# Optimization experiments

Measured on AMD Instinct MI355X. Metric: run time of the kernel, lower is better.

The kernel has to match this reference:

```python
import jax, jax.numpy as jnp
import numpy as np

D_FEAT = 6
T = 64
HID = 128
N = 8192
EPS = 1e-5


def setup_inputs() -> dict:
    key = jax.random.key(0)
    ks = jax.random.split(key, 16)
    s = 0.08
    rn = lambda k, shape: jax.random.normal(k, shape, dtype=jnp.float32) * s
    return {
        "x": jax.random.normal(ks[0], (N, D_FEAT * T), dtype=jnp.float32),
        "w_ih0": rn(ks[1], (3 * HID, D_FEAT)),
        "w_hh0": rn(ks[2], (3 * HID, HID)),
        "b_ih0": rn(ks[3], (3 * HID,)),
        "b_hh0": rn(ks[4], (3 * HID,)),
        "w_ih1": rn(ks[5], (3 * HID, HID)),
        "w_hh1": rn(ks[6], (3 * HID, HID)),
        "b_ih1": rn(ks[7], (3 * HID,)),
        "b_hh1": rn(ks[8], (3 * HID,)),
        "bn1_g": jnp.ones((HID,), jnp.float32),
        "bn1_b": jnp.zeros((HID,), jnp.float32),
        "fc_w": rn(ks[9], (HID, HID)),
        "fc_b": rn(ks[10], (HID,)),
        "bn2_g": jnp.ones((HID,), jnp.float32),
        "bn2_b": jnp.zeros((HID,), jnp.float32),
        "fco_w": rn(ks[11], (1, HID)),
        "fco_b": rn(ks[12], (1,)),
    }


def _gru_layer(xs, w_ih, w_hh, b_ih, b_hh):
    # xs: [T, N, in] -> per-step hidden states [T, N, H] (torch nn.GRU math)
    H = w_hh.shape[1]
    gi_all = jnp.einsum('tni,gi->tng', xs, w_ih) + b_ih  # precompute input gates [T,N,3H]

    def step(h, gi):
        gh = h @ w_hh.T + b_hh
        i_r, i_z, i_n = jnp.split(gi, 3, axis=1)
        h_r, h_z, h_n = jnp.split(gh, 3, axis=1)
        r = jax.nn.sigmoid(i_r + h_r)
        z = jax.nn.sigmoid(i_z + h_z)
        n = jnp.tanh(i_n + r * h_n)
        h_new = (1.0 - z) * n + z * h
        return h_new, h_new

    h0 = jnp.zeros((xs.shape[1], H), dtype=xs.dtype)
    _, hs = jax.lax.scan(step, h0, gi_all)
    return hs


def _bn(x, g, b):
    # BatchNorm1d with track_running_stats=False: always uses batch stats
    mu = jnp.mean(x, axis=0)
    var = jnp.mean((x - mu) ** 2, axis=0)
    return (x - mu) * jax.lax.rsqrt(var + EPS) * g + b


def reference(x, w_ih0, w_hh0, b_ih0, b_hh0, w_ih1, w_hh1, b_ih1, b_hh1,
              bn1_g, bn1_b, fc_w, fc_b, bn2_g, bn2_b, fco_w, fco_b):
    n = x.shape[0]
    # reshape(N, d_feat, T).permute(0,2,1) -> time-major [T, N, d_feat] for scan
    xs = x.reshape(n, D_FEAT, T).transpose(2, 0, 1)
    h1 = _gru_layer(xs, w_ih0, w_hh0, b_ih0, b_hh0)
    h2 = _gru_layer(h1, w_ih1, w_hh1, b_ih1, b_hh1)
    hidden = _bn(h2[-1], bn1_g, bn1_b)  # [N, H]
    # cal_attention: mean_d(h_i * h_j) - mean(h_i)*mean(h_j)
    #   == (hidden @ hidden.T)/H - outer(row_means, row_means)  (exact identity)
    m = jnp.mean(hidden, axis=1)
    att = hidden @ hidden.T / jnp.float32(hidden.shape[1]) - jnp.outer(m, m)  # [N, N]
    out = att @ hidden              # [N, H]
    out = out @ fc_w.T + fc_b
    out = _bn(out, bn2_g, bn2_b)
    out = jax.nn.leaky_relu(out, 0.01)
    return (out @ fco_w.T + fco_b).squeeze(-1)  # [N]
```

## Files before the change

kernel.cpp:

```cpp
#include <hip/hip_runtime.h>

typedef unsigned short u16;
typedef short bf16x8 __attribute__((ext_vector_type(8)));
typedef float f32x4 __attribute__((ext_vector_type(4)));

#define NBATCH 8192

__device__ __forceinline__ f32x4 mfma16(bf16x8 a, bf16x8 b, f32x4 c) {
  return __builtin_amdgcn_mfma_f32_16x16x32_bf16(a, b, c, 0, 0, 0);
}
__device__ __forceinline__ u16 f2bf(float f) {
  unsigned int u = __float_as_uint(f);
  return (u16)((u + 0x7FFFu + ((u >> 16) & 1u)) >> 16);
}
__device__ __forceinline__ float bf2f(u16 h) {
  return __uint_as_float(((unsigned int)h) << 16);
}
__device__ __forceinline__ float sigm(float x) {
  return __builtin_amdgcn_rcpf(1.f + __builtin_amdgcn_exp2f(-1.44269504f * x));
}
__device__ __forceinline__ float tanh_(float x) {
  float t = __builtin_amdgcn_exp2f(2.88539008f * x);
  return 1.f - 2.f * __builtin_amdgcn_rcpf(t + 1.f);
}
__device__ __forceinline__ bf16x8 pack8(const float* p) {
  float4 a = *(const float4*)p, b = *(const float4*)(p + 4);
  bf16x8 r;
  r[0] = (short)f2bf(a.x); r[1] = (short)f2bf(a.y);
  r[2] = (short)f2bf(a.z); r[3] = (short)f2bf(a.w);
  r[4] = (short)f2bf(b.x); r[5] = (short)f2bf(b.y);
  r[6] = (short)f2bf(b.z); r[7] = (short)f2bf(b.w);
  return r;
}

__device__ __forceinline__ void step_barrier() {
  __builtin_amdgcn_sched_barrier(0);
  asm volatile("s_waitcnt lgkmcnt(0)" ::: "memory");
  __builtin_amdgcn_s_barrier();
  __builtin_amdgcn_sched_barrier(0);
}

#define A_H0B  0
#define A_XB   8192
#define A_LDS  10240

#define GRU0_STEP(RD, WR, T)                                                    \
  {                                                                             \
    if (xact && (T) < 63) {                                                     \
      u16 xh = f2bf(xv);                                                        \
      u16 xl = f2bf(xv - bf2f(xh));                                             \
      char* xw = sm + A_XB + (WR)*1024 + xm*64 + xd*2;                          \
      *(u16*)xw = xh; *(u16*)(xw + 16) = xl; *(u16*)(xw + 32) = xh;             \
      if ((T) < 62) xv = gx[(T) + 2];                                           \
    }                                                                           \
    f32x4 accr = {brzr, brzr, brzr, brzr};                                      \
    f32x4 accz = {brzz, brzz, brzz, brzz};                                      \
    f32x4 acch = {bhn0, bhn0, bhn0, bhn0};                                      \
    f32x4 acci = {bin0, bin0, bin0, bin0};                                      \
    _Pragma("unroll") for (int ki = 0; ki < 4; ++ki) {                          \
      bf16x8 a0 = *(bf16x8*)(sm + A_H0B + (RD)*4096 + arow0 + ad[ki]);          \
      accr = mfma16(a0, wr0[ki], accr);                                         \
      accz = mfma16(a0, wz0[ki], accz);                                         \
      acch = mfma16(a0, wn0[ki], acch);                                         \
    }                                                                           \
    {                                                                           \
      bf16x8 ax0 = *(bf16x8*)(sm + A_XB + (RD)*1024 + xr0);                     \
      accr = mfma16(ax0, wf0a, accr);                                           \
      accz = mfma16(ax0, wf0b, accz);                                           \
      acci = mfma16(ax0, wf0c, acci);                                           \
    }                                                                           \
    if ((T) >= 1) {       \
      uint2 gv = *(const uint2*)(sm + A_H0B + (RD)*4096 + tid*8);               \
      *(uint2*)(h0seq + (size_t)((T)-1)*2097152 + gofs) = gv;                   \
    }                                                                           \
    _Pragma("unroll") for (int r = 0; r < 4; ++r) {                             \
      float rr = sigm(accr[r]);                                                 \
      float zz = sigm(accz[r]);                                                 \
      float nn = tanh_(__builtin_fmaf(rr, acch[r], acci[r]));                   \
      float h = h0s[r]; h = __builtin_fmaf(zz, h - nn, nn); h0s[r] = h;         \
      *(u16*)(sm + A_H0B + (WR)*4096 + st[r]) = f2bf(h);                        \
    }                                                                           \
    step_barrier();                                                             \
  }

__global__ __attribute__((amdgpu_flat_work_group_size(512, 512)))
void k_gru0(const float* __restrict__ x,
            const float* __restrict__ wih0, const float* __restrict__ whh0,
            const float* __restrict__ bih0, const float* __restrict__ bhh0,
            char* __restrict__ h0seq) {
  extern __shared__ char sm[];
  const int tid = threadIdx.x;
  const int wid = tid >> 6;
  const int lane = tid & 63;
  const int lq = lane >> 4;
  const int ul = lane & 15;
  const int u  = wid * 16 + ul;
  const int n0 = blockIdx.x * 16;
  const int sx = (ul & 7) << 4;
  const int gofs = blockIdx.x * 4096 + tid * 8;

  for (int idx = tid; idx < 2560; idx += 512)
    *(float*)(sm + A_H0B + idx * 4) = 0.f;

  bf16x8 wr0[4], wz0[4], wn0[4];
#pragma unroll
  for (int ki = 0; ki < 4; ++ki) {
    wr0[ki] = pack8(whh0 + u * 128 + ki * 32 + lq * 8);
    wz0[ki] = pack8(whh0 + (128 + u) * 128 + ki * 32 + lq * 8);
    wn0[ki] = pack8(whh0 + (256 + u) * 128 + ki * 32 + lq * 8);
  }

  bf16x8 wf0a, wf0b, wf0c;
  {
    u16 t0[8] = {0,0,0,0,0,0,0,0}, t1[8] = {0,0,0,0,0,0,0,0}, t2[8] = {0,0,0,0,0,0,0,0};
    u16* ts[3] = {t0, t1, t2};
#pragma unroll
    for (int i = 0; i < 3; ++i) {
      int g = u + 128 * i;
      if (lq < 2) {
        for (int d = 0; d < 6; ++d) ts[i][d] = f2bf(wih0[g * 6 + d]);
      } else if (lq == 2) {
        for (int d = 0; d < 6; ++d) {
          float w = wih0[g * 6 + d];
          u16 h = f2bf(w);
          ts[i][d] = f2bf(w - bf2f(h));
        }
      }
    }
    wf0a = *(bf16x8*)t0; wf0b = *(bf16x8*)t1; wf0c = *(bf16x8*)t2;
  }
  const float brzr = bih0[u] + bhh0[u];
  const float brzz = bih0[u + 128] + bhh0[u + 128];
  const float bin0 = bih0[u + 256], bhn0 = bhh0[u + 256];

  int ad[4];
#pragma unroll
  for (int ki = 0; ki < 4; ++ki) ad[ki] = (ki * 64 + lq * 16) ^ sx;
  const int arow0 = ul * 256;
  const int xr0 = ul * 64 + lq * 16;
  int st[4];
#pragma unroll
  for (int r = 0; r < 4; ++r) {
    int m = lq * 4 + r;
    st[r] = m * 256 + ((u * 2) ^ ((m & 7) << 4));
  }

  float h0s[4];
#pragma unroll
  for (int r = 0; r < 4; ++r) h0s[r] = 0.f;

  const int xm = tid / 6, xd = tid - 6 * xm;
  const bool xact = tid < 96;
  const float* gx = x + (size_t)(n0 + xm) * 384 + xd * 64;

  __syncthreads();

  float xv = 0.f;
  if (xact) {
    float x0 = gx[0];
    u16 h = f2bf(x0);
    u16 l = f2bf(x0 - bf2f(h));
    char* p = sm + A_XB + xm * 64 + xd * 2;
    *(u16*)p = h; *(u16*)(p + 16) = l; *(u16*)(p + 32) = h;
    xv = gx[1];
  }
  __syncthreads();

  for (int t = 0; t < 64; t += 2) {
    GRU0_STEP(0, 1, t)
    GRU0_STEP(1, 0, t + 1)
  }
  {
    uint2 gv = *(const uint2*)(sm + A_H0B + tid * 8);
    *(uint2*)(h0seq + (size_t)63 * 2097152 + gofs) = gv;
  }
}

#define B_H0IN 0
#define B_H1B  8192
#define B_LDS  16384

#define GRU1_STEP(RD, WR, T)                                                    \
  {                                                                             \
    uint2 hvnew = {0u, 0u};                                                     \
    if ((T) < 62) hvnew = *(const uint2*)(gsrc + (size_t)((T)+2)*2097152);      \
    f32x4 accr = {brzr, brzr, brzr, brzr};                                      \
    f32x4 accz = {brzz, brzz, brzz, brzz};                                      \
    f32x4 acci = {bin1, bin1, bin1, bin1};                                      \
    f32x4 acch = {bhn1, bhn1, bhn1, bhn1};                                      \
    _Pragma("unroll") for (int ki = 0; ki < 4; ++ki) {                          \
      bf16x8 p0 = *(bf16x8*)(sm + B_H0IN + (RD)*4096 + arow0 + ad[ki]);         \
      bf16x8 q0 = *(bf16x8*)(sm + B_H1B + (RD)*4096 + arow0 + ad[ki]);          \
      accr = mfma16(p0, wih1f[0][ki], accr);                                    \
      accr = mfma16(q0, wr1[ki], accr);                                         \
      accz = mfma16(p0, wih1f[1][ki], accz);                                    \
      accz = mfma16(q0, wz1[ki], accz);                                         \
      acci = mfma16(p0, wih1f[2][ki], acci);                                    \
      acch = mfma16(q0, wn1[ki], acch);                                         \
    }                                                                           \
    if ((T) < 63) *(uint2*)(sm + B_H0IN + (WR)*4096 + tid*8) = pend;            \
    _Pragma("unroll") for (int r = 0; r < 4; ++r) {                             \
      float rr = sigm(accr[r]);                                                 \
      float zz = sigm(accz[r]);                                                 \
      float nn = tanh_(__builtin_fmaf(rr, acch[r], acci[r]));                   \
      float h = h1s[r]; h = __builtin_fmaf(zz, h - nn, nn); h1s[r] = h;         \
      *(u16*)(sm + B_H1B + (WR)*4096 + st[r]) = f2bf(h);                        \
    }                                                                           \
    step_barrier();                                                             \
    pend = hvnew;                                                               \
  }

__global__ __attribute__((amdgpu_flat_work_group_size(512, 512)))
void k_gru1(const float* __restrict__ wih1, const float* __restrict__ whh1,
            const float* __restrict__ bih1, const float* __restrict__ bhh1,
            const char* __restrict__ h0seq, float* __restrict__ hraw) {
  extern __shared__ char sm[];
  const int tid = threadIdx.x;
  const int wid = tid >> 6;
  const int lane = tid & 63;
  const int lq = lane >> 4;
  const int ul = lane & 15;
  const int u  = wid * 16 + ul;
  const int n0 = blockIdx.x * 16;
  const int sx = (ul & 7) << 4;
  const char* gsrc = h0seq + blockIdx.x * 4096 + tid * 8;

  for (int idx = tid; idx < 1024; idx += 512)
    *(float*)(sm + B_H1B + idx * 4) = 0.f;
  {
    uint2 h0v = *(const uint2*)(gsrc);
    *(uint2*)(sm + B_H0IN + tid * 8) = h0v;
  }
  uint2 pend = *(const uint2*)(gsrc + 2097152);

  bf16x8 wih1f[3][4], wr1[4], wz1[4], wn1[4];
#pragma unroll
  for (int i = 0; i < 3; ++i) {
    int g = u + 128 * i;
#pragma unroll
    for (int ki = 0; ki < 4; ++ki)
      wih1f[i][ki] = pack8(wih1 + g * 128 + ki * 32 + lq * 8);
  }
#pragma unroll
  for (int ki = 0; ki < 4; ++ki) {
    wr1[ki] = pack8(whh1 + u * 128 + ki * 32 + lq * 8);
    wz1[ki] = pack8(whh1 + (128 + u) * 128 + ki * 32 + lq * 8);
    wn1[ki] = pack8(whh1 + (256 + u) * 128 + ki * 32 + lq * 8);
  }

  const float brzr = bih1[u] + bhh1[u];
  const float brzz = bih1[u + 128] + bhh1[u + 128];
  const float bin1 = bih1[u + 256], bhn1 = bhh1[u + 256];

  int ad[4];
#pragma unroll
  for (int ki = 0; ki < 4; ++ki) ad[ki] = (ki * 64 + lq * 16) ^ sx;
  const int arow0 = ul * 256;
  int st[4];
#pragma unroll
  for (int r = 0; r < 4; ++r) {
    int m = lq * 4 + r;
    st[r] = m * 256 + ((u * 2) ^ ((m & 7) << 4));
  }

  float h1s[4];
#pragma unroll
  for (int r = 0; r < 4; ++r) h1s[r] = 0.f;

  __syncthreads();

  for (int t = 0; t < 64; t += 2) {
    GRU1_STEP(0, 1, t)
    GRU1_STEP(1, 0, t + 1)
  }

#pragma unroll
  for (int r = 0; r < 4; ++r) {
    int m = lq * 4 + r;
    hraw[(size_t)(n0 + m) * 128 + u] = h1s[r];
  }
}

__global__ void k_bn1p(const float* __restrict__ hraw, float* __restrict__ p) {
  __shared__ float s0[256], s1[256];
  int tid = threadIdx.x, b = blockIdx.x;
  int f = tid & 127, r = tid >> 7;
  float s = 0.f, q = 0.f;
  for (int n = b * 64 + r; n < b * 64 + 64; n += 2) {
    float v = hraw[(size_t)n * 128 + f];
    s += v; q += v * v;
  }
  s0[tid] = s; s1[tid] = q;
  __syncthreads();
  if (tid < 128) {
    p[b * 256 + tid] = s0[tid] + s0[tid + 128];
    p[b * 256 + 128 + tid] = s1[tid] + s1[tid + 128];
  }
}

__global__ void k_bn1r(const float* __restrict__ p, float* __restrict__ mu1,
                       float* __restrict__ rs1) {
  int f = threadIdx.x;
  float s = 0.f, q = 0.f;
  for (int b = 0; b < 128; ++b) { s += p[b * 256 + f]; q += p[b * 256 + 128 + f]; }
  float mu = s / 8192.f, var = q / 8192.f - mu * mu;
  mu1[f] = mu; rs1[f] = rsqrtf(var + 1e-5f);
}

__global__ void k_attp(const float* __restrict__ hraw, const float* __restrict__ mu1,
                       const float* __restrict__ rs1, const float* __restrict__ g1,
                       const float* __restrict__ b1, float* __restrict__ hidden,
                       float* __restrict__ mvec, float* __restrict__ gpart,
                       float* __restrict__ mhpart) {
  __shared__ float hid[64][128];
  __shared__ float mld[64];
  int tid = threadIdx.x, blk = blockIdx.x, n0 = blk * 64;
  for (int idx = tid; idx < 64 * 128; idx += 256) {
    int n = idx >> 7, f = idx & 127;
    float v = (hraw[(size_t)(n0 + n) * 128 + f] - mu1[f]) * rs1[f] * g1[f] + b1[f];
    hid[n][f] = v;
    hidden[(size_t)(n0 + n) * 128 + f] = v;
  }
  __syncthreads();
  if (tid < 64) {
    float s = 0.f;
    for (int f = 0; f < 128; ++f) s += hid[tid][f];
    s *= (1.f / 128.f);
    mld[tid] = s; mvec[n0 + tid] = s;
  }
  __syncthreads();
  int i = tid >> 1, j0 = (tid & 1) * 64;
  float acc[64];
#pragma unroll
  for (int j = 0; j < 64; ++j) acc[j] = 0.f;
  for (int n = 0; n < 64; ++n) {
    float a = hid[n][i];
#pragma unroll
    for (int j = 0; j < 64; ++j) acc[j] += a * hid[n][j0 + j];
  }
#pragma unroll
  for (int j = 0; j < 64; ++j) gpart[(size_t)blk * 16384 + i * 128 + j0 + j] = acc[j];
  if (tid < 128) {
    float s = 0.f;
    for (int n = 0; n < 64; ++n) s += mld[n] * hid[n][tid];
    mhpart[blk * 128 + tid] = s;
  }
}

__global__ void k_attfa(const float* __restrict__ gpart, const float* __restrict__ mhpart,
                        float* __restrict__ gfull, float* __restrict__ mhfull) {
  int idx = blockIdx.x * 256 + threadIdx.x;
  float s = 0.f;
  for (int b = 0; b < 128; ++b) s += gpart[(size_t)b * 16384 + idx];
  gfull[idx] = s;
  if (blockIdx.x == 0 && threadIdx.x < 128) {
    float t = 0.f;
    for (int b = 0; b < 128; ++b) t += mhpart[b * 128 + threadIdx.x];
    mhfull[threadIdx.x] = t;
  }
}

__global__ void k_attfb(const float* __restrict__ gfull, const float* __restrict__ mhfull,
                        const float* __restrict__ fcw, float* __restrict__ m2,
                        float* __restrict__ uvec) {
  int idx = blockIdx.x * 128 + threadIdx.x;
  int k = idx >> 7, j = idx & 127;
  const float4* ga = (const float4*)(gfull + k * 128);
  const float4* fb = (const float4*)(fcw + j * 128);
  float a0 = 0.f, a1 = 0.f, a2 = 0.f, a3 = 0.f;
#pragma unroll 8
  for (int f = 0; f < 32; ++f) {
    float4 a = ga[f], b = fb[f];
    a0 += a.x * b.x; a1 += a.y * b.y; a2 += a.z * b.z; a3 += a.w * b.w;
  }
  m2[idx] = (a0 + a1 + a2 + a3) * (1.f / 128.f);
  if (idx < 128) {
    float s = 0.f;
    const float* fr = fcw + idx * 128;
#pragma unroll 8
    for (int f = 0; f < 128; ++f) s += mhfull[f] * fr[f];
    uvec[idx] = s;
  }
}

__global__ void k_out2(const float* __restrict__ hidden, const float* __restrict__ mvec,
                       const float* __restrict__ m2g, const float* __restrict__ uvec,
                       const float* __restrict__ fcb, float* __restrict__ out2,
                       float* __restrict__ bn2p) {
  extern __shared__ char smo[];
  float* m2l = (float*)smo;
  float* hl = m2l + 16384;
  float* ml = hl + 4096;
  float* red = ml + 32;
  int tid = threadIdx.x, blk = blockIdx.x, n0 = blk * 32;
  for (int idx = tid; idx < 16384; idx += 256) m2l[idx] = m2g[idx];
  for (int idx = tid; idx < 4096; idx += 256) hl[idx] = hidden[(size_t)n0 * 128 + idx];
  if (tid < 32) ml[tid] = mvec[n0 + tid];
  __syncthreads();
  int j = tid & 127, rg = tid >> 7;
  float uj = uvec[j], bj = fcb[j];
  float s1 = 0.f, s2 = 0.f;
  for (int q = 0; q < 16; ++q) {
    int nl = rg * 16 + q;
    float s = bj - ml[nl] * uj;
    const float* hr = hl + nl * 128;
#pragma unroll 8
    for (int k = 0; k < 128; ++k) s += hr[k] * m2l[k * 128 + j];
    out2[(size_t)(n0 + nl) * 128 + j] = s;
    s1 += s; s2 += s * s;
  }
  red[tid] = s1; red[256 + tid] = s2;
  __syncthreads();
  if (tid < 128) {
    bn2p[blk * 256 + tid] = red[tid] + red[128 + tid];
    bn2p[blk * 256 + 128 + tid] = red[256 + tid] + red[384 + tid];
  }
}

__global__ void k_bn2(const float* __restrict__ bn2p, float* __restrict__ mu2,
                      float* __restrict__ rs2) {
  int j = threadIdx.x;
  float s = 0.f, q = 0.f;
  for (int b = 0; b < 256; ++b) {
    s += bn2p[b * 256 + j];
    q += bn2p[b * 256 + 128 + j];
  }
  float mu = s / 8192.f, var = q / 8192.f - mu * mu;
  mu2[j] = mu; rs2[j] = rsqrtf(var + 1e-5f);
}

__global__ void k_fin(const float* __restrict__ out2, const float* __restrict__ mu2,
                      const float* __restrict__ rs2, const float* __restrict__ g2,
                      const float* __restrict__ b2, const float* __restrict__ fcow,
                      const float* __restrict__ fcob, float* __restrict__ y) {
  int tid = threadIdx.x, lane = tid & 63, w = tid >> 6;
  int n = blockIdx.x * 4 + w;
  float s = 0.f;
#pragma unroll
  for (int h = 0; h < 2; ++h) {
    int j = lane + h * 64;
    float v = (out2[(size_t)n * 128 + j] - mu2[j]) * rs2[j] * g2[j] + b2[j];
    v = fmaxf(v, 0.01f * v);
    s += v * fcow[j];
  }
  for (int off = 32; off; off >>= 1) s += __shfl_down(s, off);
  if (!lane) y[n] = s + fcob[0];
}

extern "C" void kernel_launch(void* const* d_in, const int* in_sizes, int n_in,
                              void* d_out, int out_size, void* d_ws, size_t ws_size,
                              hipStream_t stream) {
  const float* x    = (const float*)d_in[0];
  const float* wih0 = (const float*)d_in[1];
  const float* whh0 = (const float*)d_in[2];
  const float* bih0 = (const float*)d_in[3];
  const float* bhh0 = (const float*)d_in[4];
  const float* wih1 = (const float*)d_in[5];
  const float* whh1 = (const float*)d_in[6];
  const float* bih1 = (const float*)d_in[7];
  const float* bhh1 = (const float*)d_in[8];
  const float* g1   = (const float*)d_in[9];
  const float* b1   = (const float*)d_in[10];
  const float* fcw  = (const float*)d_in[11];
  const float* fcb  = (const float*)d_in[12];
  const float* g2   = (const float*)d_in[13];
  const float* b2   = (const float*)d_in[14];
  const float* fcow = (const float*)d_in[15];
  const float* fcob = (const float*)d_in[16];

  char* ws = (char*)d_ws;
  float* hraw   = (float*)(ws + 0);
  float* hidden = (float*)(ws + 4194304);
  float* mvec   = (float*)(ws + 8388608);
  float* mu1    = (float*)(ws + 8421376);
  float* rs1    = (float*)(ws + 8421888);
  float* gpart  = (float*)(ws + 8422400);
  float* mhpart = (float*)(ws + 16811008);
  float* m2     = (float*)(ws + 16876544);
  float* uvec   = (float*)(ws + 16942080);
  float* out2   = (float*)(ws + 16942592);
  float* bn2p   = (float*)(ws + 21136896);
  float* mu2    = (float*)(ws + 21399040);
  float* rs2    = (float*)(ws + 21399552);
  float* gfull  = (float*)(ws + 21400064);
  float* mhfull = (float*)(ws + 21465600);
  char*  h0seq  = (char*)(ws + 21495808);

  (void)hipFuncSetAttribute((const void*)k_out2,
                            hipFuncAttributeMaxDynamicSharedMemorySize, 84096);

  k_gru0<<<512, 512, A_LDS, stream>>>(x, wih0, whh0, bih0, bhh0, h0seq);
  k_gru1<<<512, 512, B_LDS, stream>>>(wih1, whh1, bih1, bhh1, h0seq, hraw);
  k_bn1p<<<128, 256, 0, stream>>>(hraw, bn2p);
  k_bn1r<<<1, 128, 0, stream>>>(bn2p, mu1, rs1);
  k_attp<<<128, 256, 0, stream>>>(hraw, mu1, rs1, g1, b1, hidden, mvec, gpart, mhpart);
  k_attfa<<<64, 256, 0, stream>>>(gpart, mhpart, gfull, mhfull);
  k_attfb<<<128, 128, 0, stream>>>(gfull, mhfull, fcw, m2, uvec);
  k_out2<<<256, 256, 84096, stream>>>(hidden, mvec, m2, uvec, fcb, out2, bn2p);
  k_bn2<<<1, 128, 0, stream>>>(bn2p, mu2, rs2);
  k_fin<<<2048, 256, 0, stream>>>(out2, mu2, rs2, g2, b2, fcow, fcob, (float*)d_out);
}
```

Measured before the change: 332.7 us.

## Load GRU1 layer-0 inputs directly from global in MFMA layout and fuse BN1 partials

GRU0 now writes each step's hidden state to global in a row-major, de-swizzled layout, so GRU1 can load its MFMA A-operand fragments for h0 straight from global memory. This removes the LDS staging buffer, the pending-register prefetch and the LDS write each step. GRU1 also computes per-block BN1 sum and sum-of-squares partials with wave shuffles, which eliminates the separate k_bn1p pass over hraw. k_bn1r becomes a parallel reduction with one block per feature. The tradeoff is that global load latency now sits on the recurrence critical path each step, with no explicit prefetch ahead of use.

```diff
diff --git a/kernel.cpp b/kernel.cpp
--- a/kernel.cpp
+++ b/kernel.cpp
@@ -69,8 +69,8 @@
       accz = mfma16(ax0, wf0b, accz);                                           \
       acci = mfma16(ax0, wf0c, acci);                                           \
     }                                                                           \
-    if ((T) >= 1) {       \
-      uint2 gv = *(const uint2*)(sm + A_H0B + (RD)*4096 + tid*8);               \
+    if ((T) >= 1) {        \
+      uint2 gv = *(const uint2*)(sm + A_H0B + (RD)*4096 + so_lds);              \
       *(uint2*)(h0seq + (size_t)((T)-1)*2097152 + gofs) = gv;                   \
     }                                                                           \
     _Pragma("unroll") for (int r = 0; r < 4; ++r) {                             \
@@ -97,7 +97,9 @@
   const int u  = wid * 16 + ul;
   const int n0 = blockIdx.x * 16;
   const int sx = (ul & 7) << 4;
-  const int gofs = blockIdx.x * 4096 + tid * 8;
+  const int so_row = tid >> 5, so_col = (tid & 31) * 8;
+  const int so_lds = so_row * 256 + (so_col ^ ((so_row & 7) << 4));
+  const int gofs = blockIdx.x * 4096 + so_row * 256 + so_col;
 
   for (int idx = tid; idx < 2560; idx += 512)
     *(float*)(sm + A_H0B + idx * 4) = 0.f;
@@ -171,34 +173,32 @@
     GRU0_STEP(1, 0, t + 1)
   }
   {
-    uint2 gv = *(const uint2*)(sm + A_H0B + tid * 8);
+    uint2 gv = *(const uint2*)(sm + A_H0B + so_lds);
     *(uint2*)(h0seq + (size_t)63 * 2097152 + gofs) = gv;
   }
 }
 
-#define B_H0IN 0
-#define B_H1B  8192
-#define B_LDS  16384
+#define B_H1B  0
+#define B_LDS  8192
 
 #define GRU1_STEP(RD, WR, T)                                                    \
   {                                                                             \
-    uint2 hvnew = {0u, 0u};                                                     \
-    if ((T) < 62) hvnew = *(const uint2*)(gsrc + (size_t)((T)+2)*2097152);      \
     f32x4 accr = {brzr, brzr, brzr, brzr};                                      \
     f32x4 accz = {brzz, brzz, brzz, brzz};                                      \
     f32x4 acci = {bin1, bin1, bin1, bin1};                                      \
     f32x4 acch = {bhn1, bhn1, bhn1, bhn1};                                      \
     _Pragma("unroll") for (int ki = 0; ki < 4; ++ki) {                          \
-      bf16x8 p0 = *(bf16x8*)(sm + B_H0IN + (RD)*4096 + arow0 + ad[ki]);         \
       bf16x8 q0 = *(bf16x8*)(sm + B_H1B + (RD)*4096 + arow0 + ad[ki]);          \
+      accr = mfma16(q0, wr1[ki], accr);                                         \
+      accz = mfma16(q0, wz1[ki], accz);                                         \
+      acch = mfma16(q0, wn1[ki], acch);                                         \
+    }                                                                           \
+    _Pragma("unroll") for (int ki = 0; ki < 4; ++ki) {                          \
+      bf16x8 p0 = *(const bf16x8*)(gsl + (size_t)(T)*2097152 + ki*64);          \
       accr = mfma16(p0, wih1f[0][ki], accr);                                    \
-      accr = mfma16(q0, wr1[ki], accr);                                         \
       accz = mfma16(p0, wih1f[1][ki], accz);                                    \
-      accz = mfma16(q0, wz1[ki], accz);                                         \
       acci = mfma16(p0, wih1f[2][ki], acci);                                    \
-      acch = mfma16(q0, wn1[ki], acch);                                         \
-    }                                                                           \
-    if ((T) < 63) *(uint2*)(sm + B_H0IN + (WR)*4096 + tid*8) = pend;            \
+    }                                                                           \
     _Pragma("unroll") for (int r = 0; r < 4; ++r) {                             \
       float rr = sigm(accr[r]);                                                 \
       float zz = sigm(accz[r]);                                                 \
@@ -207,13 +207,13 @@
       *(u16*)(sm + B_H1B + (WR)*4096 + st[r]) = f2bf(h);                        \
     }                                                                           \
     step_barrier();                                                             \
-    pend = hvnew;                                                               \
   }
 
 __global__ __attribute__((amdgpu_flat_work_group_size(512, 512)))
 void k_gru1(const float* __restrict__ wih1, const float* __restrict__ whh1,
             const float* __restrict__ bih1, const float* __restrict__ bhh1,
-            const char* __restrict__ h0seq, float* __restrict__ hraw) {
+            const char* __restrict__ h0seq, float* __restrict__ hraw,
+            float* __restrict__ bn1part) {
   extern __shared__ char sm[];
   const int tid = threadIdx.x;
   const int wid = tid >> 6;
@@ -223,15 +223,10 @@
   const int u  = wid * 16 + ul;
   const int n0 = blockIdx.x * 16;
   const int sx = (ul & 7) << 4;
-  const char* gsrc = h0seq + blockIdx.x * 4096 + tid * 8;
+  const char* gsl = h0seq + blockIdx.x * 4096 + ul * 256 + lq * 16;
 
   for (int idx = tid; idx < 1024; idx += 512)
     *(float*)(sm + B_H1B + idx * 4) = 0.f;
-  {
-    uint2 h0v = *(const uint2*)(gsrc);
-    *(uint2*)(sm + B_H0IN + tid * 8) = h0v;
-  }
-  uint2 pend = *(const uint2*)(gsrc + 2097152);
 
   bf16x8 wih1f[3][4], wr1[4], wz1[4], wn1[4];
 #pragma unroll
@@ -279,32 +274,35 @@
     int m = lq * 4 + r;
     hraw[(size_t)(n0 + m) * 128 + u] = h1s[r];
   }
-}
-
-__global__ void k_bn1p(const float* __restrict__ hraw, float* __restrict__ p) {
-  __shared__ float s0[256], s1[256];
-  int tid = threadIdx.x, b = blockIdx.x;
-  int f = tid & 127, r = tid >> 7;
-  float s = 0.f, q = 0.f;
-  for (int n = b * 64 + r; n < b * 64 + 64; n += 2) {
-    float v = hraw[(size_t)n * 128 + f];
-    s += v; q += v * v;
-  }
-  s0[tid] = s; s1[tid] = q;
-  __syncthreads();
-  if (tid < 128) {
-    p[b * 256 + tid] = s0[tid] + s0[tid + 128];
-    p[b * 256 + 128 + tid] = s1[tid] + s1[tid + 128];
+  {
+    float s = 0.f, q = 0.f;
+#pragma unroll
+    for (int r = 0; r < 4; ++r) { s += h1s[r]; q += h1s[r] * h1s[r]; }
+    s += __shfl_xor(s, 16); q += __shfl_xor(q, 16);
+    s += __shfl_xor(s, 32); q += __shfl_xor(q, 32);
+    if (lq == 0) {
+      bn1part[blockIdx.x * 256 + u] = s;
+      bn1part[blockIdx.x * 256 + 128 + u] = q;
+    }
   }
 }
 
 __global__ void k_bn1r(const float* __restrict__ p, float* __restrict__ mu1,
                        float* __restrict__ rs1) {
-  int f = threadIdx.x;
-  float s = 0.f, q = 0.f;
-  for (int b = 0; b < 128; ++b) { s += p[b * 256 + f]; q += p[b * 256 + 128 + f]; }
-  float mu = s / 8192.f, var = q / 8192.f - mu * mu;
-  mu1[f] = mu; rs1[f] = rsqrtf(var + 1e-5f);
+  __shared__ float rs[512], rq[512];
+  int f = blockIdx.x, tid = threadIdx.x;
+  rs[tid] = p[tid * 256 + f];
+  rq[tid] = p[tid * 256 + 128 + f];
+  __syncthreads();
+  for (int off = 256; off; off >>= 1) {
+    if (tid < off) { rs[tid] += rs[tid + off]; rq[tid] += rq[tid + off]; }
+    __syncthreads();
+  }
+  if (!tid) {
+    float mu = rs[0] / 8192.f;
+    float var = rq[0] / 8192.f - mu * mu;
+    mu1[f] = mu; rs1[f] = rsqrtf(var + 1e-5f);
+  }
 }
 
 __global__ void k_attp(const float* __restrict__ hraw, const float* __restrict__ mu1,
@@ -490,9 +488,8 @@
                             hipFuncAttributeMaxDynamicSharedMemorySize, 84096);
 
   k_gru0<<<512, 512, A_LDS, stream>>>(x, wih0, whh0, bih0, bhh0, h0seq);
-  k_gru1<<<512, 512, B_LDS, stream>>>(wih1, whh1, bih1, bhh1, h0seq, hraw);
-  k_bn1p<<<128, 256, 0, stream>>>(hraw, bn2p);
-  k_bn1r<<<1, 128, 0, stream>>>(bn2p, mu1, rs1);
+  k_gru1<<<512, 512, B_LDS, stream>>>(wih1, whh1, bih1, bhh1, h0seq, hraw, gpart);
+  k_bn1r<<<128, 512, 0, stream>>>(gpart, mu1, rs1);
   k_attp<<<128, 256, 0, stream>>>(hraw, mu1, rs1, g1, b1, hidden, mvec, gpart, mhpart);
   k_attfa<<<64, 256, 0, stream>>>(gpart, mhpart, gfull, mhfull);
   k_attfb<<<128, 128, 0, stream>>>(gfull, mhfull, fcw, m2, uvec);
```

Result: slower. 409.7 us (+23.1%).
